# Performance work log

Hardware: AMD Instinct MI355X
Metric: run time of the kernel (lower is better)

The kernel has to match this reference:

```python
import jax, jax.numpy as jnp
import numpy as np

D_PAIR = 128
C = 128
EPS = 1e-5

def _ln(x, g, b):
    mu = jnp.mean(x, axis=-1, keepdims=True)
    var = jnp.var(x, axis=-1, keepdims=True)
    return (x - mu) * jax.lax.rsqrt(var + EPS) * g + b

def setup_inputs() -> dict:
    key = jax.random.key(0)
    ks = jax.random.split(key, 8)
    B, N, d, c = 1, 512, D_PAIR, C
    glorot = lambda k, fo, fi: jax.random.uniform(k, (fo, fi), jnp.float32,
                                                  -1.0, 1.0) * np.sqrt(6.0 / (fi + fo))
    return {
        "Z_raw": jax.random.normal(ks[0], (B, N, N, d), jnp.float32),
        "Z_mask_row": jnp.ones((B, N, N), jnp.float32),
        "ln1_g": jnp.ones((d,), jnp.float32),
        "ln1_b": jnp.zeros((d,), jnp.float32),
        "W_lr": glorot(ks[1], 2 * c, d),
        "b_lr": jnp.zeros((2 * c,), jnp.float32),
        "W_gate": jnp.zeros((2 * c, d), jnp.float32),   # initializer='zeros'
        "b_gate": jnp.ones((2 * c,), jnp.float32),      # bias_init=1.0
        "W_og": jnp.zeros((d, d), jnp.float32),
        "b_og": jnp.ones((d,), jnp.float32),
        "ln2_g": jnp.ones((c,), jnp.float32),
        "ln2_b": jnp.zeros((c,), jnp.float32),
        "W_out": jnp.zeros((d, d), jnp.float32),        # no bias
        "out_bias": jnp.zeros((d,), jnp.float32),
    }

def reference(Z_raw, Z_mask_row, ln1_g, ln1_b, W_lr, b_lr, W_gate, b_gate,
              W_og, b_og, ln2_g, ln2_b, W_out, out_bias):
    c = C
    Z = _ln(Z_raw, ln1_g, ln1_b)                         # [B,I,J,d]
    lr = jnp.einsum('bijd,ed->bije', Z, W_lr) + b_lr      # [B,I,J,2c]
    lr = Z_mask_row[..., None] * lr
    lr = lr * jax.nn.sigmoid(jnp.einsum('bijd,ed->bije', Z, W_gate) + b_gate)
    left, right = lr[..., :c], lr[..., c:]
    # triangle outgoing: p[b,i,j,c] = sum_k left[b,i,k,c] * right[b,j,k,c]
    p = jnp.einsum('bikc,bjkc->bijc', left, right)
    ab = jnp.einsum('bijc,ec->bije', _ln(p, ln2_g, ln2_b), W_out)
    g = jax.nn.sigmoid(jnp.einsum('bijd,ed->bije', Z, W_og) + b_og)
    # eval-mode bias_ele_dropout_residual (dropout mask = ones)
    return Z_raw + g * (ab + out_bias)
```

## Files before the change

kernel.cpp:

```cpp
#include <hip/hip_runtime.h>

#define NPOS 262144

typedef __attribute__((ext_vector_type(8))) short short8;
typedef __attribute__((ext_vector_type(4))) float f32x4;
typedef __attribute__((ext_vector_type(4))) unsigned short us4;
typedef __attribute__((ext_vector_type(4))) unsigned int u32x4;

__device__ __forceinline__ unsigned short f2bf(float f){
  unsigned u = __float_as_uint(f);
  u += 0x7fffu + ((u >> 16) & 1u);
  return (unsigned short)(u >> 16);
}
__device__ __forceinline__ float bf2f(unsigned int h){ return __uint_as_float(h << 16); }
__device__ __forceinline__ float sigm(float x){ return 1.f/(1.f + __expf(-x)); }

#define MFMA16(a,b,c) __builtin_amdgcn_mfma_f32_16x16x32_bf16((a),(b),(c),0,0,0)

__global__ __launch_bounds__(256) void k_prep(
    const float* __restrict__ Wlr, const float* __restrict__ b_lr,
    const float* __restrict__ Wg,  const float* __restrict__ b_g,
    const float* __restrict__ Wog, const float* __restrict__ b_og,
    const float* __restrict__ Wout,const float* __restrict__ obias,
    const float* __restrict__ g1, const float* __restrict__ b1,
    const float* __restrict__ g2, const float* __restrict__ b2,
    unsigned short* __restrict__ Wc, float* __restrict__ svec, float* __restrict__ cvec)
{
  int r = blockIdx.x*4 + (threadIdx.x >> 6);
  int l = threadIdx.x & 63;
  const float *W, *gv, *bv; float extra;
  if (r < 256)      { W = Wlr + r*128;         extra = b_lr[r];      gv=g1; bv=b1; }
  else if (r < 512) { W = Wg  + (r-256)*128;   extra = b_g[r-256];   gv=g1; bv=b1; }
  else if (r < 640) { W = Wog + (r-512)*128;   extra = b_og[r-512];  gv=g1; bv=b1; }
  else              { W = Wout+ (r-640)*128;   extra = obias[r-640]; gv=g2; bv=b2; }
  float w0 = W[2*l], w1 = W[2*l+1];
  float p0 = w0 * gv[2*l], p1 = w1 * gv[2*l+1];
  float s  = p0 + p1;
  float cc = w0 * bv[2*l] + w1 * bv[2*l+1];
  Wc[r*128 + 2*l]   = f2bf(p0);
  Wc[r*128 + 2*l+1] = f2bf(p1);
  for (int off=32; off; off>>=1){ s += __shfl_down(s, off); cc += __shfl_down(cc, off); }
  if (l == 0){ svec[r] = s; cvec[r] = cc + extra; }
}

__global__ __launch_bounds__(256) void k_proj(
    const float* __restrict__ Zraw, const float* __restrict__ Zmask,
    const unsigned short* __restrict__ Wc,
    const float* __restrict__ svec, const float* __restrict__ cvec,
    unsigned short* __restrict__ leftT, unsigned short* __restrict__ rightT)
{
  __shared__ unsigned short zt[128*144];
  __shared__ unsigned short tl[128*132];
  __shared__ float mu_s[128], rs_s[128], mask_s[128];
  __shared__ float ps[256], pss[256];
  const int t = threadIdx.x, l = t & 63, w = t >> 6;
  const int wr = w >> 1, wc = w & 1;
  const long pos0 = (long)blockIdx.x * 128;

  { const f32x4* zg = (const f32x4*)(Zraw + pos0*128);
    for (int v=0; v<16; v++){
      int f = v*256 + t, row = f>>5, c4 = f&31;
      f32x4 z = zg[f];
      us4 h; h[0]=f2bf(z[0]); h[1]=f2bf(z[1]); h[2]=f2bf(z[2]); h[3]=f2bf(z[3]);
      *(us4*)&zt[row*144 + c4*4] = h;
    }
  }
  if (t < 128) mask_s[t] = Zmask[pos0 + t];
  __syncthreads();
  {
    int sr = t & 127, hi = t >> 7;
    float s=0.f, ss=0.f;
    for (int it=hi*32; it<hi*32+32; it++){
      int c2 = (sr + it) & 63;
      unsigned u = *(const unsigned*)&zt[sr*144 + c2*2];
      float a = bf2f(u & 0xffffu), b = bf2f(u >> 16);
      s += a + b; ss += a*a + b*b;
    }
    ps[t] = s; pss[t] = ss;
  }
  __syncthreads();
  if (t < 128){
    float s = ps[t] + ps[t+128], ss = pss[t] + pss[t+128];
    float mu = s * 0.0078125f;
    float var = ss * 0.0078125f - mu*mu;
    mu_s[t] = mu; rs_s[t] = rsqrtf(var + 1e-5f);
  }
  __syncthreads();

  for (int half=0; half<2; half++){
    const unsigned short* Blr = Wc + (half*128)*128;
    const unsigned short* Bgt = Wc + (256 + half*128)*128;
    f32x4 accL[4][4], accG[4][4];
    for (int mt=0; mt<4; mt++) for (int nt=0; nt<4; nt++){
      accL[mt][nt] = (f32x4)(0.f); accG[mt][nt] = (f32x4)(0.f);
    }
    for (int ks=0; ks<4; ks++){
      const int krow = ks*32 + ((l>>4)<<3);
      short8 bl[4], bg[4];
      for (int nt=0; nt<4; nt++){
        int n = wc*64 + nt*16 + (l&15);
        bl[nt] = *(const short8*)(Blr + n*128 + krow);
        bg[nt] = *(const short8*)(Bgt + n*128 + krow);
      }
      for (int mt=0; mt<4; mt++){
        int row = wr*64 + mt*16 + (l&15);
        short8 a = *(const short8*)&zt[row*144 + krow];
        for (int nt=0; nt<4; nt++){
          accL[mt][nt] = MFMA16(a, bl[nt], accL[mt][nt]);
          accG[mt][nt] = MFMA16(a, bg[nt], accG[mt][nt]);
        }
      }
    }
    for (int mt=0; mt<4; mt++){
      int rowb = wr*64 + mt*16 + ((l>>4)<<2);
      for (int nt=0; nt<4; nt++){
        int col = wc*64 + nt*16 + (l&15);
        float sL = svec[half*128 + col],       cL = cvec[half*128 + col];
        float sG = svec[256 + half*128 + col], cG = cvec[256 + half*128 + col];
        us4 h;
        for (int r=0; r<4; r++){
          int row = rowb + r;
          float rs = rs_s[row], rm = rs*mu_s[row];
          float lrv = rs*accL[mt][nt][r] - rm*sL + cL;
          float gv  = sigm(rs*accG[mt][nt][r] - rm*sG + cG);
          h[r] = f2bf(mask_s[row] * lrv * gv);
        }
        *(us4*)&tl[col*132 + rowb] = h;
      }
    }
    __syncthreads();
    unsigned short* dst = half ? rightT : leftT;
    for (int v=0; v<32; v++){
      int f2 = v*256 + t, col = f2>>6, rp = (f2&63)<<1;
      unsigned u = *(const unsigned*)&tl[col*132 + rp];
      *(unsigned*)&dst[(long)col*NPOS + pos0 + rp] = u;
    }
    __syncthreads();
  }
}

__global__ __launch_bounds__(256) void k_tri(
    const unsigned short* __restrict__ leftT, const unsigned short* __restrict__ rightT,
    unsigned short* __restrict__ pP)
{
  __shared__ unsigned short At[128*72];
  __shared__ unsigned short Bt[128*72];
  __shared__ unsigned short pj[128*132];
  const int t = threadIdx.x, l = t & 63, w = t >> 6;
  const int wr = w >> 1, wc = w & 1;
  const int c = blockIdx.x >> 4, tile = blockIdx.x & 15;
  const int ti = (tile >> 2) << 7, tj = (tile & 3) << 7;
  const unsigned short* L = leftT  + (long)c*NPOS + (long)ti*512;
  const unsigned short* R = rightT + (long)c*NPOS + (long)tj*512;
  f32x4 acc[4][4];
  for (int mt=0; mt<4; mt++) for (int nt=0; nt<4; nt++) acc[mt][nt] = (f32x4)(0.f);
  for (int kt=0; kt<8; kt++){
    const int k0 = kt*64;
    __syncthreads();
    for (int v=0; v<4; v++){
      int f = v*256 + t, row = f>>3, kc = f&7;
      *(u32x4*)&At[row*72 + kc*8] = *(const u32x4*)(L + row*512 + k0 + kc*8);
      *(u32x4*)&Bt[row*72 + kc*8] = *(const u32x4*)(R + row*512 + k0 + kc*8);
    }
    __syncthreads();
    for (int ks2=0; ks2<2; ks2++){
      const int krow = ks2*32 + ((l>>4)<<3);
      short8 br[4];
      for (int nt=0; nt<4; nt++)
        br[nt] = *(const short8*)&Bt[(wc*64 + nt*16 + (l&15))*72 + krow];
      for (int mt=0; mt<4; mt++){
        short8 a = *(const short8*)&At[(wr*64 + mt*16 + (l&15))*72 + krow];
        for (int nt=0; nt<4; nt++)
          acc[mt][nt] = MFMA16(a, br[nt], acc[mt][nt]);
      }
    }
  }
  __syncthreads();
  for (int mt=0; mt<4; mt++){
    int rowb = wr*64 + mt*16 + ((l>>4)<<2);
    for (int nt=0; nt<4; nt++){
      int col = wc*64 + nt*16 + (l&15);
      for (int r=0; r<4; r++)
        pj[(rowb+r)*132 + col] = f2bf(acc[mt][nt][r]);
    }
  }
  __syncthreads();
  unsigned short* dst = pP + (long)c*NPOS + (long)ti*512 + tj;
  for (int v=0; v<32; v++){
    int f2 = v*256 + t, row = f2>>6, cp = (f2&63)<<1;
    unsigned u = *(const unsigned*)&pj[row*132 + cp];
    *(unsigned*)&dst[(long)row*512 + cp] = u;
  }
}

__global__ __launch_bounds__(256) void k_out(
    const float* __restrict__ Zraw, const unsigned short* __restrict__ pP,
    const unsigned short* __restrict__ Wc,
    const float* __restrict__ svec, const float* __restrict__ cvec,
    float* __restrict__ out)
{
  __shared__ unsigned short zt[128*144];
  __shared__ unsigned pt[128*65];
  __shared__ float sb[256*4];
  __shared__ float mu1s[128], rs1s[128], mu2s[128], rs2s[128];
  const int t = threadIdx.x, l = t & 63, w = t >> 6;
  const int wr = w >> 1, wc = w & 1;
  const long pos0 = (long)blockIdx.x * 128;
  const int ib = blockIdx.x >> 2, j0 = (blockIdx.x & 3) << 7;

  { const f32x4* zg = (const f32x4*)(Zraw + pos0*128);
    for (int v=0; v<16; v++){
      int f = v*256 + t, row = f>>5, c4 = f&31;
      f32x4 z = zg[f];
      us4 h; h[0]=f2bf(z[0]); h[1]=f2bf(z[1]); h[2]=f2bf(z[2]); h[3]=f2bf(z[3]);
      *(us4*)&zt[row*144 + c4*4] = h;
    }
  }
  for (int v=0; v<32; v++){
    int f = v*256 + t, cch = f>>6, j2 = f&63;
    pt[cch*65 + j2] = *(const unsigned*)&pP[(long)cch*NPOS + (long)ib*512 + j0 + 2*j2];
  }
  __syncthreads();

  {
    int sr = t & 127, hi = t >> 7;
    float s=0.f, ss=0.f;
    for (int it=hi*32; it<hi*32+32; it++){
      int c2 = (sr + it) & 63;
      unsigned u = *(const unsigned*)&zt[sr*144 + c2*2];
      float a = bf2f(u & 0xffffu), b = bf2f(u >> 16);
      s += a + b; ss += a*a + b*b;
    }
    ps_store: ;
    sb[t*4+0] = s; sb[t*4+1] = ss;
    int jp = t & 63, ch = t >> 6;
    float s0=0.f, ss0=0.f, s1=0.f, ss1=0.f;
    for (int cc=ch*32; cc<ch*32+32; cc++){
      unsigned u = pt[cc*65 + jp];
      float a = bf2f(u & 0xffffu), b = bf2f(u >> 16);
      s0 += a; ss0 += a*a; s1 += b; ss1 += b*b;
    }
    sb[t*4+2] = s0 + s1*0.f;
    __syncthreads();
    if (t < 128){
      float S = sb[t*4+0] + sb[(t+128)*4+0];
      float SS = sb[t*4+1] + sb[(t+128)*4+1];
      float mu = S*0.0078125f, var = SS*0.0078125f - mu*mu;
      mu1s[t] = mu; rs1s[t] = rsqrtf(var + 1e-5f);
    }
    __syncthreads();
    sb[t*4+0] = s0; sb[t*4+1] = ss0; sb[t*4+2] = s1; sb[t*4+3] = ss1;
    __syncthreads();
    if (t >= 128){
      int j = t - 128, jpp = j >> 1, o = j & 1;
      float S=0.f, SS=0.f;
      for (int ww=0; ww<4; ww++){
        S  += sb[(ww*64 + jpp)*4 + 2*o];
        SS += sb[(ww*64 + jpp)*4 + 2*o + 1];
      }
      float mu = S*0.0078125f, var = SS*0.0078125f - mu*mu;
      mu2s[j] = mu; rs2s[j] = rsqrtf(var + 1e-5f);
    }
  }
  __syncthreads();

  const unsigned short* W2  = Wc + 640*128;
  const unsigned short* WgB = Wc + 512*128;
  const unsigned short* pt16 = (const unsigned short*)pt;
  f32x4 acc1[4][4], acc2[4][4];
  for (int mt=0; mt<4; mt++) for (int nt=0; nt<4; nt++){
    acc1[mt][nt]=(f32x4)(0.f); acc2[mt][nt]=(f32x4)(0.f);
  }
  for (int ks=0; ks<4; ks++){
    const int krow = ks*32 + ((l>>4)<<3);
    short8 bo[4], bg[4];
    for (int nt=0; nt<4; nt++){
      int n = wc*64 + nt*16 + (l&15);
      bo[nt] = *(const short8*)(W2  + n*128 + krow);
      bg[nt] = *(const short8*)(WgB + n*128 + krow);
    }
    for (int mt=0; mt<4; mt++){
      int row = wr*64 + mt*16 + (l&15);
      short8 ap;
      #pragma unroll
      for (int m=0; m<8; m++)
        ap[m] = (short)pt16[(krow+m)*130 + row];
      short8 az = *(const short8*)&zt[row*144 + krow];
      for (int nt=0; nt<4; nt++){
        acc1[mt][nt] = MFMA16(ap, bo[nt], acc1[mt][nt]);
        acc2[mt][nt] = MFMA16(az, bg[nt], acc2[mt][nt]);
      }
    }
  }
  for (int mt=0; mt<4; mt++){
    int rowb = wr*64 + mt*16 + ((l>>4)<<2);
    for (int nt=0; nt<4; nt++){
      int col = wc*64 + nt*16 + (l&15);
      float sO = svec[640 + col], cO = cvec[640 + col];
      float sg = svec[512 + col], cg = cvec[512 + col];
      for (int r=0; r<4; r++){
        int row = rowb + r;
        float ab = rs2s[row]*acc1[mt][nt][r] - rs2s[row]*mu2s[row]*sO + cO;
        float gv = sigm(rs1s[row]*acc2[mt][nt][r] - rs1s[row]*mu1s[row]*sg + cg);
        long gidx = (pos0 + row)*128 + col;
        out[gidx] = Zraw[gidx] + gv*ab;
      }
    }
  }
}

extern "C" void kernel_launch(void* const* d_in, const int* in_sizes, int n_in,
                              void* d_out, int out_size, void* d_ws, size_t ws_size,
                              hipStream_t stream)
{
  (void)in_sizes; (void)n_in; (void)out_size; (void)ws_size;
  const float* Zraw  = (const float*)d_in[0];
  const float* Zmask = (const float*)d_in[1];
  const float* g1    = (const float*)d_in[2];
  const float* b1    = (const float*)d_in[3];
  const float* Wlr   = (const float*)d_in[4];
  const float* blr   = (const float*)d_in[5];
  const float* Wg    = (const float*)d_in[6];
  const float* bg    = (const float*)d_in[7];
  const float* Wog   = (const float*)d_in[8];
  const float* bog   = (const float*)d_in[9];
  const float* g2    = (const float*)d_in[10];
  const float* b2    = (const float*)d_in[11];
  const float* Wout  = (const float*)d_in[12];
  const float* obias = (const float*)d_in[13];

  char* ws = (char*)d_ws;
  unsigned short* leftT  = (unsigned short*)(ws);
  unsigned short* rightT = (unsigned short*)(ws + 67108864L);
  unsigned short* pP     = (unsigned short*)(ws + 134217728L);
  unsigned short* Wc     = (unsigned short*)(ws + 201326592L);
  float* svec            = (float*)(ws + 201326592L + 196608L);
  float* cvec            = (float*)(ws + 201326592L + 196608L + 4096L);
  float* out = (float*)d_out;

  k_prep<<<192, 256, 0, stream>>>(Wlr, blr, Wg, bg, Wog, bog, Wout, obias,
                                  g1, b1, g2, b2, Wc, svec, cvec);
  k_proj<<<2048, 256, 0, stream>>>(Zraw, Zmask, Wc, svec, cvec, leftT, rightT);
  k_tri<<<2048, 256, 0, stream>>>(leftT, rightT, pP);
  k_out<<<2048, 256, 0, stream>>>(Zraw, pP, Wc, svec, cvec, out);
}
```

Baseline: 600.2 us.

## Restructure projection kernel for occupancy and compute LN stats from fp32 loads

The projection kernel now loads all Z values into registers up front. It computes the layernorm mean and variance directly from the fp32 values with wave shuffles, instead of a separate LDS pass with two barriers. The N dimension is split into two 32-column passes, which halves the accumulator registers and the transpose staging buffer, and launch bounds request 3 blocks per SM to raise occupancy. The trade-offs are more barriers and smaller global store bursts per pass, and the statistics now come from fp32 rather than bf16-rounded values.

```diff
diff --git a/kernel.cpp b/kernel.cpp
--- a/kernel.cpp
+++ b/kernel.cpp
@@ -43,99 +43,107 @@
   if (l == 0){ svec[r] = s; cvec[r] = cc + extra; }
 }
 
-__global__ __launch_bounds__(256) void k_proj(
+__global__ __launch_bounds__(256, 3) void k_proj(
     const float* __restrict__ Zraw, const float* __restrict__ Zmask,
     const unsigned short* __restrict__ Wc,
     const float* __restrict__ svec, const float* __restrict__ cvec,
     unsigned short* __restrict__ leftT, unsigned short* __restrict__ rightT)
 {
-  __shared__ unsigned short zt[128*144];
-  __shared__ unsigned short tl[128*132];
+  __shared__ unsigned short zt[128*136];
+  __shared__ unsigned short tlc[64*132];
   __shared__ float mu_s[128], rs_s[128], mask_s[128];
-  __shared__ float ps[256], pss[256];
   const int t = threadIdx.x, l = t & 63, w = t >> 6;
   const int wr = w >> 1, wc = w & 1;
   const long pos0 = (long)blockIdx.x * 128;
 
+  if (t < 128) mask_s[t] = Zmask[pos0 + t];
   { const f32x4* zg = (const f32x4*)(Zraw + pos0*128);
+    f32x4 zv[16];
+    #pragma unroll
+    for (int v=0; v<16; v++) zv[v] = zg[v*256 + t];
+    #pragma unroll
     for (int v=0; v<16; v++){
       int f = v*256 + t, row = f>>5, c4 = f&31;
-      f32x4 z = zg[f];
+      f32x4 z = zv[v];
       us4 h; h[0]=f2bf(z[0]); h[1]=f2bf(z[1]); h[2]=f2bf(z[2]); h[3]=f2bf(z[3]);
-      *(us4*)&zt[row*144 + c4*4] = h;
-    }
-  }
-  if (t < 128) mask_s[t] = Zmask[pos0 + t];
-  __syncthreads();
-  {
-    int sr = t & 127, hi = t >> 7;
-    float s=0.f, ss=0.f;
-    for (int it=hi*32; it<hi*32+32; it++){
-      int c2 = (sr + it) & 63;
-      unsigned u = *(const unsigned*)&zt[sr*144 + c2*2];
-      float a = bf2f(u & 0xffffu), b = bf2f(u >> 16);
-      s += a + b; ss += a*a + b*b;
-    }
-    ps[t] = s; pss[t] = ss;
-  }
-  __syncthreads();
-  if (t < 128){
-    float s = ps[t] + ps[t+128], ss = pss[t] + pss[t+128];
-    float mu = s * 0.0078125f;
-    float var = ss * 0.0078125f - mu*mu;
-    mu_s[t] = mu; rs_s[t] = rsqrtf(var + 1e-5f);
+      *(us4*)&zt[row*136 + c4*4] = h;
+      float s  = (z[0]+z[1]) + (z[2]+z[3]);
+      float ss = (z[0]*z[0]+z[1]*z[1]) + (z[2]*z[2]+z[3]*z[3]);
+      #pragma unroll
+      for (int off=16; off; off>>=1){ s += __shfl_xor(s, off); ss += __shfl_xor(ss, off); }
+      if ((l&31) == 0){
+        float mu = s * 0.0078125f;
+        float var = ss * 0.0078125f - mu*mu;
+        mu_s[row] = mu; rs_s[row] = rsqrtf(var + 1e-5f);
+      }
+    }
   }
   __syncthreads();
 
   for (int half=0; half<2; half++){
     const unsigned short* Blr = Wc + (half*128)*128;
     const unsigned short* Bgt = Wc + (256 + half*128)*128;
-    f32x4 accL[4][4], accG[4][4];
-    for (int mt=0; mt<4; mt++) for (int nt=0; nt<4; nt++){
-      accL[mt][nt] = (f32x4)(0.f); accG[mt][nt] = (f32x4)(0.f);
-    }
-    for (int ks=0; ks<4; ks++){
-      const int krow = ks*32 + ((l>>4)<<3);
-      short8 bl[4], bg[4];
-      for (int nt=0; nt<4; nt++){
-        int n = wc*64 + nt*16 + (l&15);
-        bl[nt] = *(const short8*)(Blr + n*128 + krow);
-        bg[nt] = *(const short8*)(Bgt + n*128 + krow);
-      }
-      for (int mt=0; mt<4; mt++){
-        int row = wr*64 + mt*16 + (l&15);
-        short8 a = *(const short8*)&zt[row*144 + krow];
-        for (int nt=0; nt<4; nt++){
-          accL[mt][nt] = MFMA16(a, bl[nt], accL[mt][nt]);
-          accG[mt][nt] = MFMA16(a, bg[nt], accG[mt][nt]);
+    for (int np=0; np<2; np++){
+      f32x4 accL[4][2], accG[4][2];
+      #pragma unroll
+      for (int mt=0; mt<4; mt++)
+        #pragma unroll
+        for (int nt=0; nt<2; nt++){
+          accL[mt][nt] = (f32x4)(0.f); accG[mt][nt] = (f32x4)(0.f);
         }
-      }
-    }
-    for (int mt=0; mt<4; mt++){
-      int rowb = wr*64 + mt*16 + ((l>>4)<<2);
-      for (int nt=0; nt<4; nt++){
-        int col = wc*64 + nt*16 + (l&15);
+      #pragma unroll
+      for (int ks=0; ks<4; ks++){
+        const int krow = ks*32 + ((l>>4)<<3);
+        short8 bl[2], bg[2];
+        #pragma unroll
+        for (int nt=0; nt<2; nt++){
+          int n = wc*64 + np*32 + nt*16 + (l&15);
+          bl[nt] = *(const short8*)(Blr + n*128 + krow);
+          bg[nt] = *(const short8*)(Bgt + n*128 + krow);
+        }
+        #pragma unroll
+        for (int mt=0; mt<4; mt++){
+          int row = wr*64 + mt*16 + (l&15);
+          short8 a = *(const short8*)&zt[row*136 + krow];
+          #pragma unroll
+          for (int nt=0; nt<2; nt++){
+            accL[mt][nt] = MFMA16(a, bl[nt], accL[mt][nt]);
+            accG[mt][nt] = MFMA16(a, bg[nt], accG[mt][nt]);
+          }
+        }
+      }
+      #pragma unroll
+      for (int nt=0; nt<2; nt++){
+        int col = wc*64 + np*32 + nt*16 + (l&15);
         float sL = svec[half*128 + col],       cL = cvec[half*128 + col];
         float sG = svec[256 + half*128 + col], cG = cvec[256 + half*128 + col];
-        us4 h;
-        for (int r=0; r<4; r++){
-          int row = rowb + r;
-          float rs = rs_s[row], rm = rs*mu_s[row];
-          float lrv = rs*accL[mt][nt][r] - rm*sL + cL;
-          float gv  = sigm(rs*accG[mt][nt][r] - rm*sG + cG);
-          h[r] = f2bf(mask_s[row] * lrv * gv);
+        int cc = wc*32 + nt*16 + (l&15);
+        #pragma unroll
+        for (int mt=0; mt<4; mt++){
+          int rowb = wr*64 + mt*16 + ((l>>4)<<2);
+          us4 h;
+          #pragma unroll
+          for (int r=0; r<4; r++){
+            int row = rowb + r;
+            float rs = rs_s[row], rm = rs*mu_s[row];
+            float lrv = rs*accL[mt][nt][r] - rm*sL + cL;
+            float gv  = sigm(rs*accG[mt][nt][r] - rm*sG + cG);
+            h[r] = f2bf(mask_s[row] * lrv * gv);
+          }
+          *(us4*)&tlc[cc*132 + rowb] = h;
         }
-        *(us4*)&tl[col*132 + rowb] = h;
-      }
-    }
-    __syncthreads();
-    unsigned short* dst = half ? rightT : leftT;
-    for (int v=0; v<32; v++){
-      int f2 = v*256 + t, col = f2>>6, rp = (f2&63)<<1;
-      unsigned u = *(const unsigned*)&tl[col*132 + rp];
-      *(unsigned*)&dst[(long)col*NPOS + pos0 + rp] = u;
-    }
-    __syncthreads();
+      }
+      __syncthreads();
+      unsigned short* dst = half ? rightT : leftT;
+      #pragma unroll
+      for (int v=0; v<16; v++){
+        int f2 = v*256 + t, cc = f2>>6, rp = (f2&63)<<1;
+        int col = ((cc>>5)<<6) + np*32 + (cc&31);
+        unsigned u = *(const unsigned*)&tlc[cc*132 + rp];
+        *(unsigned*)&dst[(long)col*NPOS + pos0 + rp] = u;
+      }
+      __syncthreads();
+    }
   }
 }
 
@@ -231,7 +239,6 @@
       float a = bf2f(u & 0xffffu), b = bf2f(u >> 16);
       s += a + b; ss += a*a + b*b;
     }
-    ps_store: ;
     sb[t*4+0] = s; sb[t*4+1] = ss;
     int jp = t & 63, ch = t >> 6;
     float s0=0.f, ss0=0.f, s1=0.f, ss1=0.f;
@@ -240,7 +247,6 @@
       float a = bf2f(u & 0xffffu), b = bf2f(u >> 16);
       s0 += a; ss0 += a*a; s1 += b; ss1 += b*b;
     }
-    sb[t*4+2] = s0 + s1*0.f;
     __syncthreads();
     if (t < 128){
       float S = sb[t*4+0] + sb[(t+128)*4+0];
```

Result: faster. 551.7 us (-8.1%).
